# Kernel optimization log

Hardware: AMD Instinct MI355X
Metric: run time of the kernel (lower is better)

## Reference

```python
import jax, jax.numpy as jnp
import numpy as np


def _apply_gates(iou, c_in):
    # iou: [..., 3H]; c_in: [..., H]  (TreeLSTMCell.apply_node_func)
    i, o, u = jnp.split(iou, 3, axis=-1)
    c = jax.nn.sigmoid(i) * jnp.tanh(u) + c_in
    h = jax.nn.sigmoid(o) * jnp.tanh(c)
    return h, c


def setup_inputs() -> dict:
    key = jax.random.key(0)
    ks = jax.random.split(key, 10)
    V, X, H, C = 32000, 300, 256, 5
    B, L = 64, 2048  # 64 perfect binary trees, 2048 leaves each
    s = lambda n: 1.0 / np.sqrt(n)
    return {
        "wordid": jax.random.randint(ks[0], (B, L), 0, V),
        "emb": jax.random.normal(ks[1], (V, X), jnp.float32) * 0.1,
        "W_iou": jax.random.normal(ks[2], (X, 3 * H), jnp.float32) * s(X),
        "b_Wiou": jnp.zeros((3 * H,), jnp.float32),
        "U_iou": jax.random.normal(ks[3], (2 * H, 3 * H), jnp.float32) * s(2 * H),
        "b_Uiou": jnp.zeros((3 * H,), jnp.float32),
        "U_f": jax.random.normal(ks[4], (2 * H, 2 * H), jnp.float32) * s(2 * H),
        "b_Uf": jnp.zeros((2 * H,), jnp.float32),
        "W_out": jax.random.normal(ks[5], (H, C), jnp.float32) * s(H),
        "b_out": jnp.zeros((C,), jnp.float32),
    }


def reference(wordid, emb, W_iou, b_Wiou, U_iou, b_Uiou, U_f, b_Uf, W_out, b_out):
    B, L = wordid.shape
    H = W_out.shape[0]
    # --- leaves: x = W_iou(embed(word)); initial c = 0 ---
    x = emb[wordid]                               # [B, L, X] gather
    iou = x @ W_iou + b_Wiou                      # [B, L, 3H]
    h, c = _apply_gates(iou, jnp.zeros((B, L, H), iou.dtype))
    h_levels = [h.reshape(B * L, H)]
    n = L
    # --- propagate up the tree (topological levels) ---
    while n > 1:
        n //= 2
        h_cat = h.reshape(B, n, 2 * H)            # concat(left,right) per parent
        c_pair = c.reshape(B, n, 2, H)
        f = jax.nn.sigmoid(h_cat @ U_f + b_Uf).reshape(B, n, 2, H)
        c_f = jnp.sum(f * c_pair, axis=2)         # [B, n, H]
        iou = h_cat @ U_iou + b_Uiou              # [B, n, 3H]
        h, c = _apply_gates(iou, c_f)
        h_levels.append(h.reshape(B * n, H))
    h_all = jnp.concatenate(h_levels, axis=0)     # [N_total, H] (level-major)
    # dropout is identity in eval mode
    return h_all @ W_out + b_out                  # [N_total, num_classes]
```

## Files before the change

kernel.cpp:

```cpp
#include <hip/hip_runtime.h>
#include <hip/hip_bf16.h>

typedef __attribute__((ext_vector_type(8))) short bfrag8;
typedef __attribute__((ext_vector_type(4))) float f32x4;

#define DIV_UP(a,b) (((a)+(b)-1)/(b))

__device__ __forceinline__ float sigm(float x){ return 1.0f/(1.0f + __expf(-x)); }
__device__ __forceinline__ float fast_tanh(float x){
  float ax = fabsf(x);
  float t = __expf(-2.0f*ax);
  float r = (1.0f - t)/(1.0f + t);
  return copysignf(r, x);
}
__device__ __forceinline__ float bf2f(short s){
  unsigned int u = ((unsigned int)(unsigned short)s) << 16;
  return __uint_as_float(u);
}
__device__ __forceinline__ unsigned short f2bf_bits(float x){
  __hip_bfloat16 b = __float2bfloat16(x);
  return *reinterpret_cast<unsigned short*>(&b);
}

#define GLOAD_LDS16(g, l) \
  __builtin_amdgcn_global_load_lds((const __attribute__((address_space(1))) void*)(g), \
                                   (__attribute__((address_space(3))) void*)(l), 16, 0, 0)

__global__ void conv_all(const float* __restrict__ emb, const float* __restrict__ Wf,
                         const float* __restrict__ Ui, const float* __restrict__ Uf,
                         __hip_bfloat16* __restrict__ oemb, __hip_bfloat16* __restrict__ owiou,
                         __hip_bfloat16* __restrict__ oucat){
  int idx = blockIdx.x*256 + threadIdx.x;
  if (idx < 32000*80) {
    int v = idx / 80, c = idx - v*80;
    ushort4 r;
    if (c < 75) {
      float4 f = *(const float4*)(emb + (size_t)v*300 + c*4);
      r.x = f2bf_bits(f.x); r.y = f2bf_bits(f.y); r.z = f2bf_bits(f.z); r.w = f2bf_bits(f.w);
    } else { r.x = r.y = r.z = r.w = 0; }
    *(ushort4*)((unsigned short*)oemb + (size_t)v*320 + c*4) = r;
    return;
  }
  idx -= 32000*80;
  if (idx < 768*320) {
    int n = idx / 320, k = idx - n*320;
    int eg = n / 48, rem = n - eg*48, gate = rem >> 4, es = rem & 15;
    int e = eg*16 + es;
    owiou[(size_t)n*320 + k] = __float2bfloat16(k < 300 ? Wf[(size_t)k*768 + gate*256 + e] : 0.0f);
    return;
  }
  idx -= 768*320;
  if (idx < 1280*512) {
    int n = idx >> 9, k = idx & 511;
    int eg = n / 80, rem = n - eg*80, gate = rem >> 4, es = rem & 15;
    int e = eg*16 + es;
    float v = (gate < 3) ? Ui[(size_t)k*768 + gate*256 + e]
                         : Uf[(size_t)k*512 + (gate-3)*256 + e];
    oucat[(size_t)n*512 + k] = __float2bfloat16(v);
  }
}

template<int NG, bool G2>
__global__ __launch_bounds__(256, 3) void gemm_fused(
    const char* __restrict__ Ab,
    const int*  __restrict__ wid,
    const char* __restrict__ Btb,
    int M, int K, int Kb,
    const float* __restrict__ b_iou,
    const float* __restrict__ b_f,
    const float* __restrict__ cprev,
    __hip_bfloat16* __restrict__ Hout, float* __restrict__ Cout)
{
  constexpr int GW  = NG*16;
  constexpr int BN  = 2*GW;
  constexpr int BCH = BN*4;
  constexpr int BUF = 8192 + BN*64;
  __shared__ __align__(16) char lds[2*BUF];

  const int lx = blockIdx.y & 7;
  const int ly = ((blockIdx.y >> 3) << 3) | (blockIdx.x & 7);
  const int row0 = ly*128;
  if (row0 >= M) return;

  const int t = threadIdx.x, lane = t & 63, w = t >> 6;
  const int wr = w >> 1, wc = w & 1;
  const int frow = lane & 15, g = lane >> 4;
  const size_t colbase = (size_t)lx * BN;
  const size_t Kbyt = (size_t)K*2;

  const char* abase0[2]; const char* abase1[2];
  #pragma unroll
  for (int i = 0; i < 2; ++i) {
    int c = t + i*256;
    int rp = c >> 3, lc = (c & 7) ^ (rp & 7);
    int r = rp*2 + (lc >> 2), q = lc & 3;
    int row = row0 + r; row = row < M ? row : M-1;
    if constexpr (G2) {
      abase0[i] = Ab + (size_t)wid[2*row]  *512 + q*16;
      abase1[i] = Ab + (size_t)wid[2*row+1]*512 + q*16 - 512;
    } else {
      abase0[i] = Ab + (size_t)row*Kb + q*16;
      abase1[i] = abase0[i];
    }
  }
  const char* bbase[3];
  const int nb = (t < 128) ? ((NG==5) ? 3 : 2) : ((NG==5) ? 2 : 1);
  #pragma unroll
  for (int i = 0; i < 3; ++i) {
    int cb = t + i*256;
    if (cb < BCH) {
      int rp = cb >> 3, lc = (cb & 7) ^ (rp & 7);
      int r = rp*2 + (lc >> 2), q = lc & 3;
      bbase[i] = Btb + (colbase + r)*Kbyt + q*16;
    } else bbase[i] = Btb;
  }

  auto STAGE = [&](int b, int ks){
    const int kb0 = ks*64;
    char* la = lds + b*BUF;
    char* lb = la + 8192;
    #pragma unroll
    for (int i = 0; i < 2; ++i) {
      const char* s = (G2 && kb0 >= 512) ? abase1[i] + kb0 : abase0[i] + kb0;
      GLOAD_LDS16(s, la + (t + i*256)*16);
    }
    #pragma unroll
    for (int i = 0; i < 3; ++i)
      if (i < nb) GLOAD_LDS16(bbase[i] + kb0, lb + (t + i*256)*16);
  };

  const int fr2 = frow >> 1;
  const int pc  = (((frow & 1)*4 + g) ^ (fr2 & 7));
  const int aoff = wr*4096 + fr2*128 + pc*16;
  const int boff = wc*(GW*64) + fr2*128 + pc*16;

  f32x4 acc[4][NG] = {};
  const int nsteps = K >> 5;

  STAGE(0, 0);
  for (int ks = 0; ks < nsteps; ++ks) {
    const int b = ks & 1;
    if (ks + 1 < nsteps) {
      STAGE(b ^ 1, ks + 1);
      if constexpr (NG == 5) {
        if (w < 2) asm volatile("s_waitcnt vmcnt(5)" ::: "memory");
        else       asm volatile("s_waitcnt vmcnt(4)" ::: "memory");
      } else {
        if (w < 2) asm volatile("s_waitcnt vmcnt(4)" ::: "memory");
        else       asm volatile("s_waitcnt vmcnt(3)" ::: "memory");
      }
    } else {
      asm volatile("s_waitcnt vmcnt(0)" ::: "memory");
    }
    __builtin_amdgcn_s_barrier();
    asm volatile("" ::: "memory");

    const char* la = lds + b*BUF;
    const char* lb = la + 8192;
    bfrag8 af[4], bfv[NG];
    #pragma unroll
    for (int mi = 0; mi < 4; ++mi) af[mi] = *(const bfrag8*)(la + aoff + mi*1024);
    #pragma unroll
    for (int gi = 0; gi < NG; ++gi) bfv[gi] = *(const bfrag8*)(lb + boff + gi*1024);
    #pragma unroll
    for (int mi = 0; mi < 4; ++mi)
      #pragma unroll
      for (int gi = 0; gi < NG; ++gi)
        acc[mi][gi] = __builtin_amdgcn_mfma_f32_16x16x32_bf16(af[mi], bfv[gi], acc[mi][gi], 0, 0, 0);

    asm volatile("" ::: "memory");
    __builtin_amdgcn_s_barrier();
  }

  const int e = lx*32 + wc*16 + frow;
  const float bi = b_iou[e], bo = b_iou[256+e], bu = b_iou[512+e];
  float bf0 = 0.f, bf1 = 0.f;
  if constexpr (NG == 5) { bf0 = b_f[e]; bf1 = b_f[256+e]; }
  #pragma unroll
  for (int mi = 0; mi < 4; ++mi) {
    const int mb = row0 + wr*64 + mi*16 + g*4;
    #pragma unroll
    for (int r = 0; r < 4; ++r) {
      const int m = mb + r;
      if (m < M) {
        float cv = sigm(acc[mi][0][r] + bi) * fast_tanh(acc[mi][2][r] + bu);
        if constexpr (NG == 5) {
          const size_t c0i = G2 ? (size_t)wid[2*m]   : (size_t)(2*m);
          const size_t c1i = G2 ? (size_t)wid[2*m+1] : (size_t)(2*m+1);
          cv += sigm(acc[mi][3][r] + bf0) * cprev[c0i*256 + e]
              + sigm(acc[mi][4][r] + bf1) * cprev[c1i*256 + e];
        }
        Cout[(size_t)m*256 + e] = cv;
        Hout[(size_t)m*256 + e] = __float2bfloat16(sigm(acc[mi][1][r] + bo) * fast_tanh(cv));
      }
    }
  }
}

__global__ void outproj_v(const __hip_bfloat16* __restrict__ h, int M,
                          const float* __restrict__ Wout, const float* __restrict__ bout,
                          float* __restrict__ out){
  const int t = threadIdx.x;
  const int half = t >> 5, l32 = t & 31;
  const int e0 = l32 * 8;
  float wv[8][5];
  #pragma unroll
  for (int j = 0; j < 8; ++j)
    #pragma unroll
    for (int cl = 0; cl < 5; ++cl) wv[j][cl] = Wout[(e0+j)*5 + cl];
  const float b0 = bout[0], b1 = bout[1], b2 = bout[2], b3 = bout[3], b4 = bout[4];
  for (int row = blockIdx.x*8 + half; row < M; row += gridDim.x*8) {
    bfrag8 hv = *(const bfrag8*)((const short*)h + (size_t)row*256 + e0);
    float a0=0,a1=0,a2=0,a3=0,a4=0;
    #pragma unroll
    for (int j = 0; j < 8; ++j) {
      float x = bf2f(hv[j]);
      a0 += x*wv[j][0]; a1 += x*wv[j][1]; a2 += x*wv[j][2]; a3 += x*wv[j][3]; a4 += x*wv[j][4];
    }
    #pragma unroll
    for (int off = 16; off; off >>= 1) {
      a0 += __shfl_down(a0, off); a1 += __shfl_down(a1, off);
      a2 += __shfl_down(a2, off); a3 += __shfl_down(a3, off); a4 += __shfl_down(a4, off);
    }
    if (l32 == 0) {
      float* op = out + (size_t)row*5;
      op[0]=a0+b0; op[1]=a1+b1; op[2]=a2+b2; op[3]=a3+b3; op[4]=a4+b4;
    }
  }
}

__global__ void leaf_scatter(const int* __restrict__ wid, const float* __restrict__ outvoc,
                             float* __restrict__ out){
  int p = blockIdx.x*256 + threadIdx.x;
  if (p >= 131072) return;
  const float* s = outvoc + (size_t)wid[p]*5;
  float* d = out + (size_t)p*5;
  #pragma unroll
  for (int j = 0; j < 5; ++j) d[j] = s[j];
}

extern "C" void kernel_launch(void* const* d_in, const int* in_sizes, int n_in,
                              void* d_out, int out_size, void* d_ws, size_t ws_size,
                              hipStream_t stream) {
  const int* wordid   = (const int*)d_in[0];
  const float* emb    = (const float*)d_in[1];
  const float* W_iou  = (const float*)d_in[2];
  const float* b_Wiou = (const float*)d_in[3];
  const float* U_iou  = (const float*)d_in[4];
  const float* b_Uiou = (const float*)d_in[5];
  const float* U_f    = (const float*)d_in[6];
  const float* b_Uf   = (const float*)d_in[7];
  const float* W_out  = (const float*)d_in[8];
  const float* b_out  = (const float*)d_in[9];
  float* out = (float*)d_out;

  char* p = (char*)d_ws;
  auto take = [&](size_t bytes){ char* r = p; p += (bytes + 255) & ~(size_t)255; return r; };
  __hip_bfloat16* wiouT  = (__hip_bfloat16*)take((size_t)768*320*2);
  __hip_bfloat16* ucatT  = (__hip_bfloat16*)take((size_t)1280*512*2);
  __hip_bfloat16* h_voc  = (__hip_bfloat16*)take((size_t)32000*256*2);
  float*          c_voc  = (float*)take((size_t)32000*256*4);
  float*          outvoc = (float*)take((size_t)32000*5*4);
  __hip_bfloat16* hAll   = (__hip_bfloat16*)take((size_t)131008*256*2);
  float*          cA     = (float*)take((size_t)65536*256*4);
  float*          cB     = (float*)take((size_t)32768*256*4);
  __hip_bfloat16* embbf  = (__hip_bfloat16*)cA;

  auto ceil8 = [](int y){ return (y + 7) & ~7; };

  const int convN = 32000*80 + 768*320 + 1280*512;
  conv_all<<<DIV_UP(convN,256),256,0,stream>>>(emb, W_iou, U_iou, U_f, embbf, wiouT, ucatT);

  gemm_fused<3,false><<<dim3(8,ceil8(250)),256,0,stream>>>(
      (const char*)embbf, nullptr, (const char*)wiouT, 32000, 320, 640,
      b_Wiou, nullptr, nullptr, h_voc, c_voc);
  outproj_v<<<1024,256,0,stream>>>(h_voc, 32000, W_out, b_out, outvoc);
  leaf_scatter<<<DIV_UP(131072,256),256,0,stream>>>(wordid, outvoc, out);

  gemm_fused<5,true><<<dim3(8,512),256,0,stream>>>(
      (const char*)h_voc, wordid, (const char*)ucatT, 65536, 512, 0,
      b_Uiou, b_Uf, c_voc, hAll, cA);

  const __hip_bfloat16* hp = hAll; const float* cp = cA;
  size_t hoff = 65536;
  int Mlvl = 65536;
  for (int lvl = 2; lvl <= 11; ++lvl) {
    Mlvl >>= 1;
    float* cn = (lvl & 1) ? cA : cB;
    gemm_fused<5,false><<<dim3(8,ceil8(DIV_UP(Mlvl,128))),256,0,stream>>>(
        (const char*)hp, nullptr, (const char*)ucatT, Mlvl, 512, 1024,
        b_Uiou, b_Uf, cp, hAll + hoff*256, cn);
    hp = hAll + hoff*256; cp = cn; hoff += Mlvl;
  }

  outproj_v<<<2048,256,0,stream>>>(hAll, 131008, W_out, b_out, out + (size_t)131072*5);
}
```

Measured before the change: 475.2 us.

## Add 256x160-tile GEMM kernel for the three largest tree levels

```diff
diff --git a/kernel.cpp b/kernel.cpp
--- a/kernel.cpp
+++ b/kernel.cpp
@@ -62,12 +62,9 @@
 
 template<int NG, bool G2>
 __global__ __launch_bounds__(256, 3) void gemm_fused(
-    const char* __restrict__ Ab,
-    const int*  __restrict__ wid,
-    const char* __restrict__ Btb,
-    int M, int K, int Kb,
-    const float* __restrict__ b_iou,
-    const float* __restrict__ b_f,
+    const char* __restrict__ Ab, const int* __restrict__ wid,
+    const char* __restrict__ Btb, int M, int K, int Kb,
+    const float* __restrict__ b_iou, const float* __restrict__ b_f,
     const float* __restrict__ cprev,
     __hip_bfloat16* __restrict__ Hout, float* __restrict__ Cout)
 {
@@ -197,6 +194,132 @@
   }
 }
 
+template<bool G2>
+__global__ __launch_bounds__(512, 2) void gemm_big(
+    const char* __restrict__ Ab, const int* __restrict__ wid,
+    const char* __restrict__ Btb, int M, int Kb,
+    const float* __restrict__ b_iou, const float* __restrict__ b_f,
+    const float* __restrict__ cprev,
+    __hip_bfloat16* __restrict__ Hout, float* __restrict__ Cout)
+{
+  constexpr int K   = 512;
+  constexpr int BUF = 53248;
+  __shared__ __align__(16) char lds[2*BUF];
+
+  const int lx = blockIdx.y & 7;
+  const int ly = ((blockIdx.y >> 3) << 3) | (blockIdx.x & 7);
+  const int row0 = ly*256;
+  if (row0 >= M) return;
+
+  const int t = threadIdx.x, lane = t & 63, w = t >> 6;
+  const int wr = w >> 1, wc = w & 1;
+  const int frow = lane & 15, g = lane >> 4;
+  const size_t colbase = (size_t)lx * 160;
+  const size_t Kbyt = (size_t)K*2;
+
+  const char* abase0[2]; const char* abase1[2];
+  #pragma unroll
+  for (int i = 0; i < 2; ++i) {
+    int c = t + i*512;
+    int rp = c >> 3, lc = (c & 7) ^ (rp & 7);
+    int r = rp*2 + (lc >> 2), q = lc & 3;
+    int row = row0 + r; row = row < M ? row : M-1;
+    if constexpr (G2) {
+      abase0[i] = Ab + (size_t)wid[2*row]  *512 + q*16;
+      abase1[i] = Ab + (size_t)wid[2*row+1]*512 + q*16 - 512;
+    } else {
+      abase0[i] = Ab + (size_t)row*Kb + q*16;
+      abase1[i] = abase0[i];
+    }
+  }
+  const char* bbase[2];
+  const int nbB = (t < 128) ? 2 : 1;
+  #pragma unroll
+  for (int i = 0; i < 2; ++i) {
+    int cb = t + i*512;
+    if (cb < 640) {
+      int rp = cb >> 3, lc = (cb & 7) ^ (rp & 7);
+      int r = rp*2 + (lc >> 2), q = lc & 3;
+      bbase[i] = Btb + (colbase + r)*Kbyt + q*16;
+    } else bbase[i] = Btb;
+  }
+
+  auto STAGE = [&](int p, int tau){
+    const int kb = tau*128;
+    char* base = lds + p*BUF;
+    #pragma unroll
+    for (int h = 0; h < 2; ++h) {
+      const int kb0 = kb + h*64;
+      #pragma unroll
+      for (int i = 0; i < 2; ++i) {
+        const char* s = (G2 && kb0 >= 512) ? abase1[i] + kb0 : abase0[i] + kb0;
+        GLOAD_LDS16(s, base + h*16384 + (t + i*512)*16);
+      }
+      #pragma unroll
+      for (int i = 0; i < 2; ++i)
+        if (i < nbB) GLOAD_LDS16(bbase[i] + kb0, base + 32768 + h*10240 + (t + i*512)*16);
+    }
+  };
+
+  const int fr2 = frow >> 1;
+  const int pc  = (((frow & 1)*4 + g) ^ (fr2 & 7));
+  const int aoff = wr*4096 + fr2*128 + pc*16;
+  const int boff = wc*5120 + fr2*128 + pc*16;
+
+  f32x4 acc[4][5] = {};
+
+  STAGE(0, 0);
+  for (int tau = 0; tau < 8; ++tau) {
+    const int p = tau & 1;
+    asm volatile("s_waitcnt vmcnt(0)" ::: "memory");
+    __builtin_amdgcn_s_barrier();
+    asm volatile("" ::: "memory");
+    if (tau + 1 < 8) STAGE(p ^ 1, tau + 1);
+
+    const char* base = lds + p*BUF;
+    bfrag8 bfv[2][5];
+    #pragma unroll
+    for (int h = 0; h < 2; ++h)
+      #pragma unroll
+      for (int gi = 0; gi < 5; ++gi)
+        bfv[h][gi] = *(const bfrag8*)(base + 32768 + h*10240 + boff + gi*1024);
+
+    __builtin_amdgcn_s_setprio(1);
+    #pragma unroll
+    for (int mi = 0; mi < 4; ++mi) {
+      bfrag8 a0 = *(const bfrag8*)(base + aoff + mi*1024);
+      bfrag8 a1 = *(const bfrag8*)(base + 16384 + aoff + mi*1024);
+      #pragma unroll
+      for (int gi = 0; gi < 5; ++gi) {
+        acc[mi][gi] = __builtin_amdgcn_mfma_f32_16x16x32_bf16(a0, bfv[0][gi], acc[mi][gi], 0, 0, 0);
+        acc[mi][gi] = __builtin_amdgcn_mfma_f32_16x16x32_bf16(a1, bfv[1][gi], acc[mi][gi], 0, 0, 0);
+      }
+    }
+    __builtin_amdgcn_s_setprio(0);
+  }
+
+  const int e = lx*32 + wc*16 + frow;
+  const float bi = b_iou[e], bo = b_iou[256+e], bu = b_iou[512+e];
+  const float bf0 = b_f[e], bf1 = b_f[256+e];
+  #pragma unroll
+  for (int mi = 0; mi < 4; ++mi) {
+    const int mb = row0 + wr*64 + mi*16 + g*4;
+    #pragma unroll
+    for (int r = 0; r < 4; ++r) {
+      const int m = mb + r;
+      if (m < M) {
+        const size_t c0i = G2 ? (size_t)wid[2*m]   : (size_t)(2*m);
+        const size_t c1i = G2 ? (size_t)wid[2*m+1] : (size_t)(2*m+1);
+        float cv = sigm(acc[mi][0][r] + bi) * fast_tanh(acc[mi][2][r] + bu)
+                 + sigm(acc[mi][3][r] + bf0) * cprev[c0i*256 + e]
+                 + sigm(acc[mi][4][r] + bf1) * cprev[c1i*256 + e];
+        Cout[(size_t)m*256 + e] = cv;
+        Hout[(size_t)m*256 + e] = __float2bfloat16(sigm(acc[mi][1][r] + bo) * fast_tanh(cv));
+      }
+    }
+  }
+}
+
 __global__ void outproj_v(const __hip_bfloat16* __restrict__ h, int M,
                           const float* __restrict__ Wout, const float* __restrict__ bout,
                           float* __restrict__ out){
@@ -277,14 +400,21 @@
   outproj_v<<<1024,256,0,stream>>>(h_voc, 32000, W_out, b_out, outvoc);
   leaf_scatter<<<DIV_UP(131072,256),256,0,stream>>>(wordid, outvoc, out);
 
-  gemm_fused<5,true><<<dim3(8,512),256,0,stream>>>(
-      (const char*)h_voc, wordid, (const char*)ucatT, 65536, 512, 0,
+  gemm_big<true><<<dim3(8,ceil8(DIV_UP(65536,256))),512,0,stream>>>(
+      (const char*)h_voc, wordid, (const char*)ucatT, 65536, 0,
       b_Uiou, b_Uf, c_voc, hAll, cA);
-
-  const __hip_bfloat16* hp = hAll; const float* cp = cA;
-  size_t hoff = 65536;
-  int Mlvl = 65536;
-  for (int lvl = 2; lvl <= 11; ++lvl) {
+  gemm_big<false><<<dim3(8,ceil8(DIV_UP(32768,256))),512,0,stream>>>(
+      (const char*)hAll, nullptr, (const char*)ucatT, 32768, 1024,
+      b_Uiou, b_Uf, cA, hAll + (size_t)65536*256, cB);
+  gemm_big<false><<<dim3(8,ceil8(DIV_UP(16384,256))),512,0,stream>>>(
+      (const char*)(hAll + (size_t)65536*256), nullptr, (const char*)ucatT, 16384, 1024,
+      b_Uiou, b_Uf, cB, hAll + (size_t)98304*256, cA);
+
+  const __hip_bfloat16* hp = hAll + (size_t)98304*256;
+  const float* cp = cA;
+  size_t hoff = 114688;
+  int Mlvl = 16384;
+  for (int lvl = 4; lvl <= 11; ++lvl) {
     Mlvl >>= 1;
     float* cn = (lvl & 1) ? cA : cB;
     gemm_fused<5,false><<<dim3(8,ceil8(DIV_UP(Mlvl,128))),256,0,stream>>>(
```

Measured after the change: 526.5 us. 10.8% more time.
